# Optimization experiments

Hardware: AMD Instinct MI355X
Metric: run time of the kernel (lower is better)

## Reference

```python
import jax, jax.numpy as jnp
import numpy as np

N = 4096           # batch size (square similarity matrix)
NUM_BINS = 10      # histogram bins (module default)
NUM_CLASSES = 64   # classes used to synthesize the relevance matrix


def setup_inputs() -> dict:
    key = jax.random.key(0)
    k1, k2 = jax.random.split(key)
    # cosine similarities in [-1, 1]
    batch = jax.random.uniform(k1, (N, N), jnp.float32, -1.0, 1.0)
    # relevance matrix from class labels: labels[i,j] = 1 if same class
    cls = jax.random.randint(k2, (N,), 0, NUM_CLASSES)
    labels = (cls[:, None] == cls[None, :]).astype(jnp.float32)
    return {"batch": batch, "labels": labels}


def reference(batch, labels):
    num_bins = NUM_BINS
    I_pos = labels
    I_neg = 1.0 - labels
    N_pos = jnp.sum(labels, axis=1)                      # [N]
    dist2 = 2.0 - 2.0 * jnp.clip(batch, -1.0, 1.0)       # [N, N], in [0, 4]
    Delta = 4.0 / num_bins
    Z = jnp.linspace(0.0, 4.0, num_bins + 1)             # [L], L = num_bins+1

    # soft binning pulse for all bins at once: [N, N, L]
    pulse = jnp.maximum(0.0, 1.0 - jnp.abs(dist2[..., None] - Z) / Delta)
    h_pos = jnp.einsum('nml,nm->nl', pulse, I_pos)       # [N, L]
    h_neg = jnp.einsum('nml,nm->nl', pulse, I_neg)       # [N, L]

    H_pos = jnp.cumsum(h_pos, axis=1)
    H = jnp.cumsum(h_pos + h_neg, axis=1)

    # FastAP = h_pos * H_pos / H, with nan/inf (H == 0) set to 0
    safe_H = jnp.where(H > 0, H, 1.0)
    ap_terms = jnp.where(H > 0, h_pos * H_pos / safe_H, 0.0)

    safe_Np = jnp.where(N_pos > 0, N_pos, 1.0)
    ap = jnp.sum(ap_terms, axis=1) / safe_Np             # [N]

    # drop NaN rows (N_pos == 0) from the mean, matching FastAP[~isnan]
    valid = N_pos > 0
    mean_ap = jnp.sum(jnp.where(valid, ap, 0.0)) / jnp.sum(valid.astype(ap.dtype))
    return 1.0 - mean_ap
```

## Files before the change

kernel.cpp:

```cpp
#include <hip/hip_runtime.h>

#define N 4096
#define NBINS 10
#define BLOCK 256
#define F4T (N / 4 / BLOCK)
#define NSLOTS 64

__global__ __launch_bounds__(BLOCK) void fastap_cid_kernel(
    const float* __restrict__ labels, int* __restrict__ cid,
    float* __restrict__ slots)
{
    if (blockIdx.x == 0 && threadIdx.x < NSLOTS)
        slots[threadIdx.x * 16] = 0.f;

    const int lane = threadIdx.x & 63;
    const int wid  = (blockIdx.x * BLOCK + threadIdx.x) >> 6;
    #pragma unroll
    for (int rr = 0; rr < 4; ++rr) {
        const int row = wid * 4 + rr;
        const float4* l4 = (const float4*)(labels + (size_t)row * N);
        bool done = false;
        for (int r = 0; !done; ++r) {
            float4 v = l4[r * 64 + lane];
            bool any = (v.x > 0.5f) || (v.y > 0.5f) || (v.z > 0.5f) || (v.w > 0.5f);
            unsigned long long m = __ballot(any);
            if (m) {
                int fl = __builtin_ctzll(m);
                if (lane == fl) {
                    int e = (v.x > 0.5f) ? 0 : (v.y > 0.5f) ? 1 : (v.z > 0.5f) ? 2 : 3;
                    cid[row] = r * 256 + lane * 4 + e;
                }
                done = true;
            }
        }
    }
}

__global__ __launch_bounds__(BLOCK) void fastap_row_kernel(
    const float* __restrict__ batch, const int* __restrict__ cid,
    float* __restrict__ slots)
{
    const int tid  = threadIdx.x;
    const int lane = tid & 63;
    const int wave = tid >> 6;
    const int row  = blockIdx.x;

    const float4* b4 = (const float4*)(batch + (size_t)row * N);
    const int4*   c4 = (const int4*)cid;
    const int myc = cid[row];

    float4 bv[F4T]; int4 cv[F4T];
    #pragma unroll
    for (int i = 0; i < F4T; ++i) {
        bv[i] = b4[i * BLOCK + tid];
        cv[i] = c4[i * BLOCK + tid];
    }

    float hc_pos[NBINS], hc_all[NBINS], np = 0.f;
    #pragma unroll
    for (int l = 0; l < NBINS; ++l) { hc_pos[l] = 0.f; hc_all[l] = 0.f; }

    #pragma unroll
    for (int i = 0; i < F4T; ++i) {
        #pragma unroll
        for (int e = 0; e < 4; ++e) {
            float x   = ((const float*)&bv[i])[e];
            float lbl = (((const int*)&cv[i])[e] == myc) ? 1.f : 0.f;
            float u = fmaf(5.f, x, -4.f);
            np += lbl;
            #pragma unroll
            for (int l = 0; l < NBINS; ++l) {
                float c = fminf(fmaxf(u + (float)l, 0.f), 1.f);
                hc_pos[l] = fmaf(c, lbl, hc_pos[l]);
                hc_all[l] += c;
            }
        }
    }

    #pragma unroll
    for (int off = 1; off < 64; off <<= 1) {
        #pragma unroll
        for (int l = 0; l < NBINS; ++l) {
            hc_pos[l] += __shfl_xor(hc_pos[l], off, 64);
            hc_all[l] += __shfl_xor(hc_all[l], off, 64);
        }
        np += __shfl_xor(np, off, 64);
    }

    __shared__ float s[4][2 * NBINS + 1];
    if (lane == 0) {
        #pragma unroll
        for (int l = 0; l < NBINS; ++l) {
            s[wave][l]         = hc_pos[l];
            s[wave][NBINS + l] = hc_all[l];
        }
        s[wave][2 * NBINS] = np;
    }
    __syncthreads();

    if (tid == 0) {
        float Hp_prev = 0.f, ap = 0.f;
        #pragma unroll
        for (int l = 0; l < NBINS; ++l) {
            float Hp = s[0][l] + s[1][l] + s[2][l] + s[3][l];
            float Ha = s[0][NBINS + l] + s[1][NBINS + l]
                     + s[2][NBINS + l] + s[3][NBINS + l];
            float hp = Hp - Hp_prev;
            if (Ha > 0.f) ap += hp * Hp / Ha;
            Hp_prev = Hp;
        }
        float Np = s[0][2 * NBINS] + s[1][2 * NBINS]
                 + s[2][2 * NBINS] + s[3][2 * NBINS];
        ap += (Np - Hp_prev) * Np * (1.f / (float)N);
        atomicAdd(&slots[(row & (NSLOTS - 1)) * 16], ap / Np);
    }
}

__global__ void fastap_finalize(const float* __restrict__ slots,
                                float* __restrict__ out)
{
    const int lane = threadIdx.x;
    float v = slots[lane * 16];
    #pragma unroll
    for (int off = 32; off > 0; off >>= 1)
        v += __shfl_down(v, off, 64);
    if (lane == 0) out[0] = 1.f - v * (1.f / (float)N);
}

extern "C" void kernel_launch(void* const* d_in, const int* in_sizes, int n_in,
                              void* d_out, int out_size, void* d_ws, size_t ws_size,
                              hipStream_t stream) {
    const float* batch  = (const float*)d_in[0];
    const float* labels = (const float*)d_in[1];
    int*   cid   = (int*)d_ws;
    float* slots = (float*)(cid + N);
    fastap_cid_kernel<<<N / (4 * 4), BLOCK, 0, stream>>>(labels, cid, slots);
    fastap_row_kernel<<<N, BLOCK, 0, stream>>>(batch, cid, slots);
    fastap_finalize<<<1, 64, 0, stream>>>(slots, (float*)d_out);
}
```

Before: 146.5 us.

## Assign one row per wave with double-buffered loads and 16-bit class ids

The row kernel now maps each 64-lane wave to a full row instead of a 256-thread block per row, processing the row in four groups with a double-buffered prefetch of the next group. This removes the shared-memory cross-wave reduction and block barrier. Class ids are stored as 16-bit values to halve their read traffic. The trade-off is more serial work and register pressure per thread, and each wave rereads the whole class-id array.

```diff
diff --git a/kernel.cpp b/kernel.cpp
--- a/kernel.cpp
+++ b/kernel.cpp
@@ -3,11 +3,12 @@
 #define N 4096
 #define NBINS 10
 #define BLOCK 256
-#define F4T (N / 4 / BLOCK)
 #define NSLOTS 64
+#define GROUPS 4
+#define GF4 4
 
 __global__ __launch_bounds__(BLOCK) void fastap_cid_kernel(
-    const float* __restrict__ labels, int* __restrict__ cid,
+    const float* __restrict__ labels, unsigned short* __restrict__ cid,
     float* __restrict__ slots)
 {
     if (blockIdx.x == 0 && threadIdx.x < NSLOTS)
@@ -28,7 +29,7 @@
                 int fl = __builtin_ctzll(m);
                 if (lane == fl) {
                     int e = (v.x > 0.5f) ? 0 : (v.y > 0.5f) ? 1 : (v.z > 0.5f) ? 2 : 3;
-                    cid[row] = r * 256 + lane * 4 + e;
+                    cid[row] = (unsigned short)(r * 256 + lane * 4 + e);
                 }
                 done = true;
             }
@@ -37,42 +38,52 @@
 }
 
 __global__ __launch_bounds__(BLOCK) void fastap_row_kernel(
-    const float* __restrict__ batch, const int* __restrict__ cid,
+    const float* __restrict__ batch, const unsigned short* __restrict__ cid,
     float* __restrict__ slots)
 {
     const int tid  = threadIdx.x;
     const int lane = tid & 63;
-    const int wave = tid >> 6;
-    const int row  = blockIdx.x;
+    const int row  = (blockIdx.x * BLOCK + tid) >> 6;
 
-    const float4* b4 = (const float4*)(batch + (size_t)row * N);
-    const int4*   c4 = (const int4*)cid;
+    const float4*  b4 = (const float4*)(batch + (size_t)row * N);
+    const ushort4* c4 = (const ushort4*)cid;
     const int myc = cid[row];
-
-    float4 bv[F4T]; int4 cv[F4T];
-    #pragma unroll
-    for (int i = 0; i < F4T; ++i) {
-        bv[i] = b4[i * BLOCK + tid];
-        cv[i] = c4[i * BLOCK + tid];
-    }
 
     float hc_pos[NBINS], hc_all[NBINS], np = 0.f;
     #pragma unroll
     for (int l = 0; l < NBINS; ++l) { hc_pos[l] = 0.f; hc_all[l] = 0.f; }
 
+    float4 buf[2][GF4];
     #pragma unroll
-    for (int i = 0; i < F4T; ++i) {
+    for (int i = 0; i < GF4; ++i) buf[0][i] = b4[i * 64 + lane];
+
+    #pragma unroll
+    for (int g = 0; g < GROUPS; ++g) {
+        const int cb = g & 1;
+        if (g + 1 < GROUPS) {
+            #pragma unroll
+            for (int i = 0; i < GF4; ++i)
+                buf[(g + 1) & 1][i] = b4[((g + 1) * GF4 + i) * 64 + lane];
+        }
+        ushort4 cv[GF4];
         #pragma unroll
-        for (int e = 0; e < 4; ++e) {
-            float x   = ((const float*)&bv[i])[e];
-            float lbl = (((const int*)&cv[i])[e] == myc) ? 1.f : 0.f;
-            float u = fmaf(5.f, x, -4.f);
-            np += lbl;
+        for (int i = 0; i < GF4; ++i) cv[i] = c4[(g * GF4 + i) * 64 + lane];
+
+        #pragma unroll
+        for (int i = 0; i < GF4; ++i) {
             #pragma unroll
-            for (int l = 0; l < NBINS; ++l) {
-                float c = fminf(fmaxf(u + (float)l, 0.f), 1.f);
-                hc_pos[l] = fmaf(c, lbl, hc_pos[l]);
-                hc_all[l] += c;
+            for (int e = 0; e < 4; ++e) {
+                float x  = ((const float*)&buf[cb][i])[e];
+                int   cc = ((const unsigned short*)&cv[i])[e];
+                float lbl = (cc == myc) ? 1.f : 0.f;
+                float u = fmaf(5.f, x, -4.f);
+                np += lbl;
+                #pragma unroll
+                for (int l = 0; l < NBINS; ++l) {
+                    float c = fminf(fmaxf(u + (float)l, 0.f), 1.f);
+                    hc_pos[l] = fmaf(c, lbl, hc_pos[l]);
+                    hc_all[l] += c;
+                }
             }
         }
     }
@@ -87,30 +98,17 @@
         np += __shfl_xor(np, off, 64);
     }
 
-    __shared__ float s[4][2 * NBINS + 1];
     if (lane == 0) {
-        #pragma unroll
-        for (int l = 0; l < NBINS; ++l) {
-            s[wave][l]         = hc_pos[l];
-            s[wave][NBINS + l] = hc_all[l];
-        }
-        s[wave][2 * NBINS] = np;
-    }
-    __syncthreads();
-
-    if (tid == 0) {
         float Hp_prev = 0.f, ap = 0.f;
         #pragma unroll
         for (int l = 0; l < NBINS; ++l) {
-            float Hp = s[0][l] + s[1][l] + s[2][l] + s[3][l];
-            float Ha = s[0][NBINS + l] + s[1][NBINS + l]
-                     + s[2][NBINS + l] + s[3][NBINS + l];
+            float Hp = hc_pos[l];
+            float Ha = hc_all[l];
             float hp = Hp - Hp_prev;
             if (Ha > 0.f) ap += hp * Hp / Ha;
             Hp_prev = Hp;
         }
-        float Np = s[0][2 * NBINS] + s[1][2 * NBINS]
-                 + s[2][2 * NBINS] + s[3][2 * NBINS];
+        float Np = np;
         ap += (Np - Hp_prev) * Np * (1.f / (float)N);
         atomicAdd(&slots[(row & (NSLOTS - 1)) * 16], ap / Np);
     }
@@ -132,9 +130,9 @@
                               hipStream_t stream) {
     const float* batch  = (const float*)d_in[0];
     const float* labels = (const float*)d_in[1];
-    int*   cid   = (int*)d_ws;
-    float* slots = (float*)(cid + N);
+    unsigned short* cid = (unsigned short*)d_ws;
+    float* slots = (float*)((char*)d_ws + 8192);
     fastap_cid_kernel<<<N / (4 * 4), BLOCK, 0, stream>>>(labels, cid, slots);
-    fastap_row_kernel<<<N, BLOCK, 0, stream>>>(batch, cid, slots);
+    fastap_row_kernel<<<N / 4, BLOCK, 0, stream>>>(batch, cid, slots);
     fastap_finalize<<<1, 64, 0, stream>>>(slots, (float*)d_out);
 }
```

After: 142.5 us. -2.7%, faster.
